# Kernel tuning notes

Hardware: AMD Instinct MI355X
Metric: run time of the kernel (lower is better)

Reference implementation:

```python
import jax, jax.numpy as jnp
import numpy as np

ALPHA = 0.5
E_MINUS_1 = float(np.e - 1.0)  # exp(1) - 1; exp(0) - 1 == 0

B = 4096
CLASSES = [128, 512, 2048, 8192]


def _ce(logits, labels):
    # mean cross-entropy: -mean(log_softmax(logits)[i, labels[i]])
    logp = jax.nn.log_softmax(logits, axis=-1)
    nll = -jnp.take_along_axis(logp, labels[:, None], axis=-1)[:, 0]
    return jnp.mean(nll)


def setup_inputs() -> dict:
    key = jax.random.key(0)
    ks = jax.random.split(key, 12)
    inp = {}
    for l, c in enumerate(CLASSES):
        inp[f"out{l}"] = jax.random.normal(ks[l], (B, c), dtype=jnp.float32)
    # targets[:, l] must be < CLASSES[l]; keep all < min(CLASSES) for simplicity
    inp["targets"] = jax.random.randint(ks[4], (B, 4), 0, 128).astype(jnp.int64)
    for l, c in enumerate(CLASSES):
        inp[f"pred{l}"] = jax.random.randint(ks[5 + l], (B,), 0, c).astype(jnp.int64)
    inp["valid01"] = jax.random.randint(ks[9], (128, 512), 0, 2).astype(bool)
    inp["valid12"] = jax.random.randint(ks[10], (512, 2048), 0, 2).astype(bool)
    inp["valid23"] = jax.random.randint(ks[11], (2048, 8192), 0, 2).astype(bool)
    return inp


def reference(out0, out1, out2, out3, targets, pred0, pred1, pred2, pred3,
              valid01, valid12, valid23):
    outputs = [out0, out1, out2, out3]
    preds = [pred0, pred1, pred2, pred3]
    valids = [valid01, valid12, valid23]

    total_ce = sum(_ce(outputs[l], targets[:, l]) for l in range(len(outputs)))

    # dependency loss: per sample, exp(D)-1 with D=0 if (prev_pred -> curr_pred)
    # is a valid parent-child pair, else D=1; averaged over batch, summed over levels
    total_dep = jnp.zeros((), dtype=out0.dtype)
    for l, V in enumerate(valids):
        ok = V[preds[l], preds[l + 1]]  # [B] bool gather (vectorized dict lookup)
        total_dep = total_dep + E_MINUS_1 * jnp.mean(1.0 - ok.astype(out0.dtype))

    total = ALPHA * total_ce + (1.0 - ALPHA) * total_dep
    return (total, total_ce, total_dep)
```

## Files before the change

### kernel.cpp

```cpp
#include <hip/hip_runtime.h>
#include <float.h>


#define NB 4096

static constexpr float LOG2E = 1.4426950408889634f;
static constexpr float LN2   = 0.6931471805599453f;
static constexpr float E_M1  = 1.7182818284590452f;

__device__ __forceinline__ float hw_exp2(float x) { return __builtin_amdgcn_exp2f(x); }
__device__ __forceinline__ float hw_log2(float x) { return __builtin_amdgcn_logf(x); }

__device__ __forceinline__ float wave_max(float v) {
    #pragma unroll
    for (int off = 32; off; off >>= 1) v = fmaxf(v, __shfl_xor(v, off));
    return v;
}
__device__ __forceinline__ float wave_sum(float v) {
    #pragma unroll
    for (int off = 32; off; off >>= 1) v += __shfl_xor(v, off);
    return v;
}
__device__ __forceinline__ float max4(float4 v) {
    return fmaxf(fmaxf(v.x, v.y), fmaxf(v.z, v.w));
}
__device__ __forceinline__ float sumexp4(float4 v, float M) {
    return hw_exp2((v.x - M) * LOG2E) + hw_exp2((v.y - M) * LOG2E)
         + hw_exp2((v.z - M) * LOG2E) + hw_exp2((v.w - M) * LOG2E);
}

__global__ __launch_bounds__(256) void ce_fused_kernel(
    const float* __restrict__ o0, const float* __restrict__ o1,
    const float* __restrict__ o2, const float* __restrict__ o3,
    const int* __restrict__ targets,
    const int* __restrict__ p0, const int* __restrict__ p1,
    const int* __restrict__ p2, const int* __restrict__ p3,
    const int* __restrict__ v01, const int* __restrict__ v12,
    const int* __restrict__ v23, float* __restrict__ ws8)
{
    const int row  = blockIdx.x;
    const int tid  = threadIdx.x;
    const int wv   = tid >> 6;
    const int lane = tid & 63;

    int ia = 0, ib = 0, ic = 0, id = 0;
    if (tid == 192) {
        ia = p0[row]; ib = p1[row]; ic = p2[row]; id = p3[row];
    }

    const float4* r3 = (const float4*)(o3 + (size_t)row * 8192);
    float4 v3[8];
    #pragma unroll
    for (int k = 0; k < 8; k++) v3[k] = r3[tid + (k << 8)];

    const float4* r0 = (const float4*)(o0 + (size_t)row * 128);
    const float4* r1 = (const float4*)(o1 + (size_t)row * 512);
    const float4* r2 = (const float4*)(o2 + (size_t)row * 2048);
    float4 vs[4];
    if (wv == 0) {
        if (lane < 32) vs[0] = r0[lane];
    } else if (wv == 1) {
        vs[0] = r1[lane];
        vs[1] = r1[lane + 64];
    } else {
        const int t2 = tid - 128;
        #pragma unroll
        for (int j = 0; j < 4; j++) vs[j] = r2[t2 + j * 128];
    }

    if (tid == 192) {
        const float ok0 = (v01[ia * 512  + ib] != 0) ? 1.f : 0.f;
        const float ok1 = (v12[ib * 2048 + ic] != 0) ? 1.f : 0.f;
        const float ok2 = (v23[ic * 8192 + id] != 0) ? 1.f : 0.f;
        ws8[row * 8 + 4] = ok0;
        ws8[row * 8 + 5] = ok1;
        ws8[row * 8 + 6] = ok2;
    }

    float xt_a = 0.0f, xt_b = 0.0f;
    if (tid == 0) {
        xt_a = o3[(size_t)row * 8192 + targets[row * 4 + 3]];
        xt_b = o0[(size_t)row * 128  + targets[row * 4 + 0]];
    } else if (tid == 64) {
        xt_a = o1[(size_t)row * 512  + targets[row * 4 + 1]];
    } else if (tid == 128) {
        xt_a = o2[(size_t)row * 2048 + targets[row * 4 + 2]];
    }

    __shared__ float lm3[4], lm2[2], ls3[4], ls2[2];

    float m3 = -FLT_MAX;
    #pragma unroll
    for (int k = 0; k < 8; k++) m3 = fmaxf(m3, max4(v3[k]));
    m3 = wave_max(m3);

    float msml = -FLT_MAX;
    if (wv == 0) {
        if (lane < 32) msml = max4(vs[0]);
    } else if (wv == 1) {
        msml = fmaxf(max4(vs[0]), max4(vs[1]));
    } else {
        #pragma unroll
        for (int j = 0; j < 4; j++) msml = fmaxf(msml, max4(vs[j]));
    }
    msml = wave_max(msml);

    if (lane == 0) {
        lm3[wv] = m3;
        if (wv >= 2) lm2[wv - 2] = msml;
    }
    __syncthreads();

    const float M3 = fmaxf(fmaxf(lm3[0], lm3[1]), fmaxf(lm3[2], lm3[3]));
    const float M2 = (wv >= 2) ? fmaxf(lm2[0], lm2[1]) : 0.0f;

    float s3 = 0.0f;
    #pragma unroll
    for (int k = 0; k < 8; k++) s3 += sumexp4(v3[k], M3);
    s3 = wave_sum(s3);

    float ssml = 0.0f;
    if (wv == 0) {
        if (lane < 32) ssml = sumexp4(vs[0], msml);
    } else if (wv == 1) {
        ssml = sumexp4(vs[0], msml) + sumexp4(vs[1], msml);
    } else {
        #pragma unroll
        for (int j = 0; j < 4; j++) ssml += sumexp4(vs[j], M2);
    }
    ssml = wave_sum(ssml);

    if (lane == 0) {
        ls3[wv] = s3;
        if (wv >= 2) ls2[wv - 2] = ssml;
    }
    __syncthreads();

    if (tid == 0) {
        const float S3 = ls3[0] + ls3[1] + ls3[2] + ls3[3];
        ws8[row * 8 + 3] = M3 + hw_log2(S3) * LN2 - xt_a;
        ws8[row * 8 + 0] = msml + hw_log2(ssml) * LN2 - xt_b;
    } else if (tid == 64) {
        ws8[row * 8 + 1] = msml + hw_log2(ssml) * LN2 - xt_a;
    } else if (tid == 128) {
        const float S2 = ls2[0] + ls2[1];
        ws8[row * 8 + 2] = M2 + hw_log2(S2) * LN2 - xt_a;
    }
}

__global__ __launch_bounds__(1024) void finalize_kernel(
    const float* __restrict__ ws8, float* __restrict__ out)
{
    const int tid = threadIdx.x;
    const float4* w4 = (const float4*)ws8;

    float c0 = 0.f, c1 = 0.f, c2 = 0.f, c3 = 0.f;
    float ok0 = 0.f, ok1 = 0.f, ok2 = 0.f;
    #pragma unroll
    for (int j = 0; j < 4; j++) {
        const int row = tid + j * 1024;
        float4 a = w4[row * 2];
        float4 b = w4[row * 2 + 1];
        c0 += a.x; c1 += a.y; c2 += a.z; c3 += a.w;
        ok0 += b.x; ok1 += b.y; ok2 += b.z;
    }

    float vals[7] = {c0, c1, c2, c3, ok0, ok1, ok2};
    #pragma unroll
    for (int q = 0; q < 7; q++) {
        #pragma unroll
        for (int off = 32; off; off >>= 1) vals[q] += __shfl_xor(vals[q], off);
    }
    __shared__ float lds[16][7];
    if ((tid & 63) == 0) {
        #pragma unroll
        for (int q = 0; q < 7; q++) lds[tid >> 6][q] = vals[q];
    }
    __syncthreads();

    if (tid == 0) {
        float res[7];
        #pragma unroll
        for (int q = 0; q < 7; q++) {
            float t = 0.f;
            for (int w = 0; w < 16; w++) t += lds[w][q];
            res[q] = t;
        }
        const float inv_b = 1.0f / (float)NB;
        const float total_ce = (res[0] + res[1] + res[2] + res[3]) * inv_b;
        float total_dep = 0.f;
        #pragma unroll
        for (int q = 4; q < 7; q++)
            total_dep += E_M1 * (((float)NB - res[q]) * inv_b);
        out[0] = 0.5f * total_ce + 0.5f * total_dep;
        out[1] = total_ce;
        out[2] = total_dep;
    }
}

extern "C" void kernel_launch(void* const* d_in, const int* in_sizes, int n_in,
                              void* d_out, int out_size, void* d_ws, size_t ws_size,
                              hipStream_t stream)
{
    const float* o0 = (const float*)d_in[0];
    const float* o1 = (const float*)d_in[1];
    const float* o2 = (const float*)d_in[2];
    const float* o3 = (const float*)d_in[3];
    const int* targets = (const int*)d_in[4];
    const int* p0 = (const int*)d_in[5];
    const int* p1 = (const int*)d_in[6];
    const int* p2 = (const int*)d_in[7];
    const int* p3 = (const int*)d_in[8];
    const int* v01 = (const int*)d_in[9];
    const int* v12 = (const int*)d_in[10];
    const int* v23 = (const int*)d_in[11];

    float* ws8 = (float*)d_ws;
    float* out = (float*)d_out;

    ce_fused_kernel<<<NB, 256, 0, stream>>>(o0, o1, o2, o3, targets,
                                            p0, p1, p2, p3, v01, v12, v23, ws8);
    finalize_kernel<<<1, 1024, 0, stream>>>(ws8, out);
}
```

Baseline: 269.5 us.

## Use online softmax with single barrier and staged row loads

Replaces the two-pass max-then-sum softmax reduction with an online (running max, rescaled sum) formulation combined across lanes, waves and the block. This removes one block barrier and halves the per-thread register buffer for the largest row by loading its second half after processing the first. It adds extra exp evaluations for rescaling and in the shuffle reductions, and the second-half loads may expose more memory latency.

```diff
diff --git a/kernel.cpp b/kernel.cpp
--- a/kernel.cpp
+++ b/kernel.cpp
@@ -11,22 +11,27 @@
 __device__ __forceinline__ float hw_exp2(float x) { return __builtin_amdgcn_exp2f(x); }
 __device__ __forceinline__ float hw_log2(float x) { return __builtin_amdgcn_logf(x); }
 
-__device__ __forceinline__ float wave_max(float v) {
-    #pragma unroll
-    for (int off = 32; off; off >>= 1) v = fmaxf(v, __shfl_xor(v, off));
-    return v;
-}
-__device__ __forceinline__ float wave_sum(float v) {
-    #pragma unroll
-    for (int off = 32; off; off >>= 1) v += __shfl_xor(v, off);
-    return v;
-}
 __device__ __forceinline__ float max4(float4 v) {
     return fmaxf(fmaxf(v.x, v.y), fmaxf(v.z, v.w));
 }
 __device__ __forceinline__ float sumexp4(float4 v, float M) {
     return hw_exp2((v.x - M) * LOG2E) + hw_exp2((v.y - M) * LOG2E)
          + hw_exp2((v.z - M) * LOG2E) + hw_exp2((v.w - M) * LOG2E);
+}
+__device__ __forceinline__ void online4(float4 v, float& m, float& s) {
+    float mn = fmaxf(m, max4(v));
+    s = s * hw_exp2((m - mn) * LOG2E) + sumexp4(v, mn);
+    m = mn;
+}
+__device__ __forceinline__ void combine_ms(float& m, float& s, float m2, float s2) {
+    float mn = fmaxf(m, m2);
+    s = s * hw_exp2((m - mn) * LOG2E) + s2 * hw_exp2((m2 - mn) * LOG2E);
+    m = mn;
+}
+__device__ __forceinline__ void wave_reduce_ms(float& m, float& s) {
+    #pragma unroll
+    for (int off = 32; off; off >>= 1)
+        combine_ms(m, s, __shfl_xor(m, off), __shfl_xor(s, off));
 }
 
 __global__ __launch_bounds__(256) void ce_fused_kernel(
@@ -49,32 +54,32 @@
     }
 
     const float4* r3 = (const float4*)(o3 + (size_t)row * 8192);
-    float4 v3[8];
-    #pragma unroll
-    for (int k = 0; k < 8; k++) v3[k] = r3[tid + (k << 8)];
+    float4 b0 = r3[tid];
+    float4 b1 = r3[tid + 256];
+    float4 b2 = r3[tid + 512];
+    float4 b3 = r3[tid + 768];
 
     const float4* r0 = (const float4*)(o0 + (size_t)row * 128);
     const float4* r1 = (const float4*)(o1 + (size_t)row * 512);
     const float4* r2 = (const float4*)(o2 + (size_t)row * 2048);
-    float4 vs[4];
+    float4 u0, u1, u2, u3;
     if (wv == 0) {
-        if (lane < 32) vs[0] = r0[lane];
+        if (lane < 32) u0 = r0[lane];
     } else if (wv == 1) {
-        vs[0] = r1[lane];
-        vs[1] = r1[lane + 64];
+        u0 = r1[lane];
+        u1 = r1[lane + 64];
     } else {
         const int t2 = tid - 128;
-        #pragma unroll
-        for (int j = 0; j < 4; j++) vs[j] = r2[t2 + j * 128];
+        u0 = r2[t2];
+        u1 = r2[t2 + 128];
+        u2 = r2[t2 + 256];
+        u3 = r2[t2 + 384];
     }
 
     if (tid == 192) {
-        const float ok0 = (v01[ia * 512  + ib] != 0) ? 1.f : 0.f;
-        const float ok1 = (v12[ib * 2048 + ic] != 0) ? 1.f : 0.f;
-        const float ok2 = (v23[ic * 8192 + id] != 0) ? 1.f : 0.f;
-        ws8[row * 8 + 4] = ok0;
-        ws8[row * 8 + 5] = ok1;
-        ws8[row * 8 + 6] = ok2;
+        ws8[row * 8 + 4] = (v01[ia * 512  + ib] != 0) ? 1.f : 0.f;
+        ws8[row * 8 + 5] = (v12[ib * 2048 + ic] != 0) ? 1.f : 0.f;
+        ws8[row * 8 + 6] = (v23[ic * 8192 + id] != 0) ? 1.f : 0.f;
     }
 
     float xt_a = 0.0f, xt_b = 0.0f;
@@ -87,64 +92,55 @@
         xt_a = o2[(size_t)row * 2048 + targets[row * 4 + 2]];
     }
 
-    __shared__ float lm3[4], lm2[2], ls3[4], ls2[2];
-
-    float m3 = -FLT_MAX;
-    #pragma unroll
-    for (int k = 0; k < 8; k++) m3 = fmaxf(m3, max4(v3[k]));
-    m3 = wave_max(m3);
-
-    float msml = -FLT_MAX;
+    float m0 = -FLT_MAX, m1 = -FLT_MAX, m2 = -FLT_MAX, m3 = -FLT_MAX;
+    float s0 = 0.f, s1 = 0.f, s2 = 0.f, s3 = 0.f;
+    online4(b0, m0, s0);  b0 = r3[tid + 1024];
+    online4(b1, m1, s1);  b1 = r3[tid + 1280];
+    online4(b2, m2, s2);  b2 = r3[tid + 1536];
+    online4(b3, m3, s3);  b3 = r3[tid + 1792];
+    online4(b0, m0, s0);
+    online4(b1, m1, s1);
+    online4(b2, m2, s2);
+    online4(b3, m3, s3);
+    combine_ms(m0, s0, m1, s1);
+    combine_ms(m2, s2, m3, s3);
+    combine_ms(m0, s0, m2, s2);
+    wave_reduce_ms(m0, s0);
+
+    float ms = -FLT_MAX, ss = 0.f;
     if (wv == 0) {
-        if (lane < 32) msml = max4(vs[0]);
+        if (lane < 32) online4(u0, ms, ss);
     } else if (wv == 1) {
-        msml = fmaxf(max4(vs[0]), max4(vs[1]));
+        online4(u0, ms, ss);
+        online4(u1, ms, ss);
     } else {
-        #pragma unroll
-        for (int j = 0; j < 4; j++) msml = fmaxf(msml, max4(vs[j]));
-    }
-    msml = wave_max(msml);
-
+        online4(u0, ms, ss);
+        online4(u1, ms, ss);
+        online4(u2, ms, ss);
+        online4(u3, ms, ss);
+    }
+    wave_reduce_ms(ms, ss);
+
+    __shared__ float lm3[4], ls3[4], lmS[2], lsS[2];
     if (lane == 0) {
-        lm3[wv] = m3;
-        if (wv >= 2) lm2[wv - 2] = msml;
+        lm3[wv] = m0; ls3[wv] = s0;
+        if (wv >= 2) { lmS[wv - 2] = ms; lsS[wv - 2] = ss; }
     }
     __syncthreads();
 
-    const float M3 = fmaxf(fmaxf(lm3[0], lm3[1]), fmaxf(lm3[2], lm3[3]));
-    const float M2 = (wv >= 2) ? fmaxf(lm2[0], lm2[1]) : 0.0f;
-
-    float s3 = 0.0f;
-    #pragma unroll
-    for (int k = 0; k < 8; k++) s3 += sumexp4(v3[k], M3);
-    s3 = wave_sum(s3);
-
-    float ssml = 0.0f;
-    if (wv == 0) {
-        if (lane < 32) ssml = sumexp4(vs[0], msml);
-    } else if (wv == 1) {
-        ssml = sumexp4(vs[0], msml) + sumexp4(vs[1], msml);
-    } else {
-        #pragma unroll
-        for (int j = 0; j < 4; j++) ssml += sumexp4(vs[j], M2);
-    }
-    ssml = wave_sum(ssml);
-
-    if (lane == 0) {
-        ls3[wv] = s3;
-        if (wv >= 2) ls2[wv - 2] = ssml;
-    }
-    __syncthreads();
-
     if (tid == 0) {
-        const float S3 = ls3[0] + ls3[1] + ls3[2] + ls3[3];
-        ws8[row * 8 + 3] = M3 + hw_log2(S3) * LN2 - xt_a;
-        ws8[row * 8 + 0] = msml + hw_log2(ssml) * LN2 - xt_b;
+        float M = lm3[0], S = ls3[0];
+        combine_ms(M, S, lm3[1], ls3[1]);
+        combine_ms(M, S, lm3[2], ls3[2]);
+        combine_ms(M, S, lm3[3], ls3[3]);
+        ws8[row * 8 + 3] = M + hw_log2(S) * LN2 - xt_a;
+        ws8[row * 8 + 0] = ms + hw_log2(ss) * LN2 - xt_b;
     } else if (tid == 64) {
-        ws8[row * 8 + 1] = msml + hw_log2(ssml) * LN2 - xt_a;
+        ws8[row * 8 + 1] = ms + hw_log2(ss) * LN2 - xt_a;
     } else if (tid == 128) {
-        const float S2 = ls2[0] + ls2[1];
-        ws8[row * 8 + 2] = M2 + hw_log2(S2) * LN2 - xt_a;
+        float M = lmS[0], S = lsS[0];
+        combine_ms(M, S, lmS[1], lsS[1]);
+        ws8[row * 8 + 2] = M + hw_log2(S) * LN2 - xt_a;
     }
 }
 
```

Result: no change. 273.8 us (+1.6%).

## Split per-row CE work into independent waves with online softmax for large rows

Applied to the files above, without the earlier changes.

The kernel no longer uses one 256-thread block per row. Each wave now handles one task: an 8192-wide row, a 2048-wide row, or the small 512 and 128 rows plus the dependency lookups. The 8192-wide rows use a single-pass online max/sum-exp with 8 independent accumulators and register double-buffered loads. This removes block-level __syncthreads and LDS reductions and aims for better load balance. In exchange, each wave streams 32 KB serially and does extra exp work for the online rescaling.

```diff
diff --git a/kernel.cpp b/kernel.cpp
--- a/kernel.cpp
+++ b/kernel.cpp
@@ -11,16 +11,6 @@
 __device__ __forceinline__ float hw_exp2(float x) { return __builtin_amdgcn_exp2f(x); }
 __device__ __forceinline__ float hw_log2(float x) { return __builtin_amdgcn_logf(x); }
 
-__device__ __forceinline__ float wave_max(float v) {
-    #pragma unroll
-    for (int off = 32; off; off >>= 1) v = fmaxf(v, __shfl_xor(v, off));
-    return v;
-}
-__device__ __forceinline__ float wave_sum(float v) {
-    #pragma unroll
-    for (int off = 32; off; off >>= 1) v += __shfl_xor(v, off);
-    return v;
-}
 __device__ __forceinline__ float max4(float4 v) {
     return fmaxf(fmaxf(v.x, v.y), fmaxf(v.z, v.w));
 }
@@ -28,8 +18,28 @@
     return hw_exp2((v.x - M) * LOG2E) + hw_exp2((v.y - M) * LOG2E)
          + hw_exp2((v.z - M) * LOG2E) + hw_exp2((v.w - M) * LOG2E);
 }
-
-__global__ __launch_bounds__(256) void ce_fused_kernel(
+__device__ __forceinline__ void online4(float4 v, float& m, float& s) {
+    float mn = fmaxf(m, max4(v));
+    s = s * hw_exp2((m - mn) * LOG2E) + sumexp4(v, mn);
+    m = mn;
+}
+__device__ __forceinline__ void combine_ms(float& m, float& s, float m2, float s2) {
+    float mn = fmaxf(m, m2);
+    s = s * hw_exp2((m - mn) * LOG2E) + s2 * hw_exp2((m2 - mn) * LOG2E);
+    m = mn;
+}
+__device__ __forceinline__ float wave_max(float v) {
+    #pragma unroll
+    for (int off = 32; off; off >>= 1) v = fmaxf(v, __shfl_xor(v, off));
+    return v;
+}
+__device__ __forceinline__ float wave_sum(float v) {
+    #pragma unroll
+    for (int off = 32; off; off >>= 1) v += __shfl_xor(v, off);
+    return v;
+}
+
+__global__ __launch_bounds__(256) void ce_wave_kernel(
     const float* __restrict__ o0, const float* __restrict__ o1,
     const float* __restrict__ o2, const float* __restrict__ o3,
     const int* __restrict__ targets,
@@ -38,113 +48,120 @@
     const int* __restrict__ v01, const int* __restrict__ v12,
     const int* __restrict__ v23, float* __restrict__ ws8)
 {
-    const int row  = blockIdx.x;
-    const int tid  = threadIdx.x;
-    const int wv   = tid >> 6;
-    const int lane = tid & 63;
-
-    int ia = 0, ib = 0, ic = 0, id = 0;
-    if (tid == 192) {
-        ia = p0[row]; ib = p1[row]; ic = p2[row]; id = p3[row];
-    }
-
-    const float4* r3 = (const float4*)(o3 + (size_t)row * 8192);
-    float4 v3[8];
-    #pragma unroll
-    for (int k = 0; k < 8; k++) v3[k] = r3[tid + (k << 8)];
-
-    const float4* r0 = (const float4*)(o0 + (size_t)row * 128);
-    const float4* r1 = (const float4*)(o1 + (size_t)row * 512);
-    const float4* r2 = (const float4*)(o2 + (size_t)row * 2048);
-    float4 vs[4];
-    if (wv == 0) {
-        if (lane < 32) vs[0] = r0[lane];
-    } else if (wv == 1) {
-        vs[0] = r1[lane];
-        vs[1] = r1[lane + 64];
+    const int gw   = (blockIdx.x << 2) | (threadIdx.x >> 6);
+    const int lane = threadIdx.x & 63;
+
+    if (gw < 4096) {
+        const int row = gw;
+        const float4* r3 = (const float4*)(o3 + (size_t)row * 8192);
+
+        int tgt = 0;
+        if (lane == 0) tgt = targets[row * 4 + 3];
+
+        float4 buf[8];
+        #pragma unroll
+        for (int j = 0; j < 8; j++) buf[j] = r3[lane + (j << 6)];
+
+        float xt = 0.0f;
+        if (lane == 0) xt = o3[(size_t)row * 8192 + tgt];
+
+        float m[8], s[8];
+        #pragma unroll
+        for (int j = 0; j < 8; j++) { m[j] = -FLT_MAX; s[j] = 0.0f; }
+
+        #pragma unroll
+        for (int r = 0; r < 3; r++) {
+            #pragma unroll
+            for (int j = 0; j < 8; j++) {
+                float4 v = buf[j];
+                buf[j] = r3[lane + (((r + 1) << 3 | j) << 6)];
+                online4(v, m[j], s[j]);
+            }
+        }
+        #pragma unroll
+        for (int j = 0; j < 8; j++) online4(buf[j], m[j], s[j]);
+
+        combine_ms(m[0], s[0], m[1], s[1]);
+        combine_ms(m[2], s[2], m[3], s[3]);
+        combine_ms(m[4], s[4], m[5], s[5]);
+        combine_ms(m[6], s[6], m[7], s[7]);
+        combine_ms(m[0], s[0], m[2], s[2]);
+        combine_ms(m[4], s[4], m[6], s[6]);
+        combine_ms(m[0], s[0], m[4], s[4]);
+        float M = m[0], S = s[0];
+        #pragma unroll
+        for (int off = 32; off; off >>= 1)
+            combine_ms(M, S, __shfl_xor(M, off), __shfl_xor(S, off));
+
+        if (lane == 0) ws8[row * 8 + 3] = M + hw_log2(S) * LN2 - xt;
+
+    } else if (gw < 8192) {
+        const int row = gw - 4096;
+        const float4* r2 = (const float4*)(o2 + (size_t)row * 2048);
+
+        int tgt = 0;
+        if (lane == 0) tgt = targets[row * 4 + 2];
+
+        float4 buf[8];
+        #pragma unroll
+        for (int j = 0; j < 8; j++) buf[j] = r2[lane + (j << 6)];
+
+        float xt = 0.0f;
+        if (lane == 0) xt = o2[(size_t)row * 2048 + tgt];
+
+        float pm = -FLT_MAX;
+        #pragma unroll
+        for (int j = 0; j < 8; j++) pm = fmaxf(pm, max4(buf[j]));
+        const float M = wave_max(pm);
+
+        float ps = 0.0f;
+        #pragma unroll
+        for (int j = 0; j < 8; j++) ps += sumexp4(buf[j], M);
+        const float S = wave_sum(ps);
+
+        if (lane == 0) ws8[row * 8 + 2] = M + hw_log2(S) * LN2 - xt;
+
     } else {
-        const int t2 = tid - 128;
-        #pragma unroll
-        for (int j = 0; j < 4; j++) vs[j] = r2[t2 + j * 128];
-    }
-
-    if (tid == 192) {
-        const float ok0 = (v01[ia * 512  + ib] != 0) ? 1.f : 0.f;
-        const float ok1 = (v12[ib * 2048 + ic] != 0) ? 1.f : 0.f;
-        const float ok2 = (v23[ic * 8192 + id] != 0) ? 1.f : 0.f;
-        ws8[row * 8 + 4] = ok0;
-        ws8[row * 8 + 5] = ok1;
-        ws8[row * 8 + 6] = ok2;
-    }
-
-    float xt_a = 0.0f, xt_b = 0.0f;
-    if (tid == 0) {
-        xt_a = o3[(size_t)row * 8192 + targets[row * 4 + 3]];
-        xt_b = o0[(size_t)row * 128  + targets[row * 4 + 0]];
-    } else if (tid == 64) {
-        xt_a = o1[(size_t)row * 512  + targets[row * 4 + 1]];
-    } else if (tid == 128) {
-        xt_a = o2[(size_t)row * 2048 + targets[row * 4 + 2]];
-    }
-
-    __shared__ float lm3[4], lm2[2], ls3[4], ls2[2];
-
-    float m3 = -FLT_MAX;
-    #pragma unroll
-    for (int k = 0; k < 8; k++) m3 = fmaxf(m3, max4(v3[k]));
-    m3 = wave_max(m3);
-
-    float msml = -FLT_MAX;
-    if (wv == 0) {
-        if (lane < 32) msml = max4(vs[0]);
-    } else if (wv == 1) {
-        msml = fmaxf(max4(vs[0]), max4(vs[1]));
-    } else {
-        #pragma unroll
-        for (int j = 0; j < 4; j++) msml = fmaxf(msml, max4(vs[j]));
-    }
-    msml = wave_max(msml);
-
-    if (lane == 0) {
-        lm3[wv] = m3;
-        if (wv >= 2) lm2[wv - 2] = msml;
-    }
-    __syncthreads();
-
-    const float M3 = fmaxf(fmaxf(lm3[0], lm3[1]), fmaxf(lm3[2], lm3[3]));
-    const float M2 = (wv >= 2) ? fmaxf(lm2[0], lm2[1]) : 0.0f;
-
-    float s3 = 0.0f;
-    #pragma unroll
-    for (int k = 0; k < 8; k++) s3 += sumexp4(v3[k], M3);
-    s3 = wave_sum(s3);
-
-    float ssml = 0.0f;
-    if (wv == 0) {
-        if (lane < 32) ssml = sumexp4(vs[0], msml);
-    } else if (wv == 1) {
-        ssml = sumexp4(vs[0], msml) + sumexp4(vs[1], msml);
-    } else {
-        #pragma unroll
-        for (int j = 0; j < 4; j++) ssml += sumexp4(vs[j], M2);
-    }
-    ssml = wave_sum(ssml);
-
-    if (lane == 0) {
-        ls3[wv] = s3;
-        if (wv >= 2) ls2[wv - 2] = ssml;
-    }
-    __syncthreads();
-
-    if (tid == 0) {
-        const float S3 = ls3[0] + ls3[1] + ls3[2] + ls3[3];
-        ws8[row * 8 + 3] = M3 + hw_log2(S3) * LN2 - xt_a;
-        ws8[row * 8 + 0] = msml + hw_log2(ssml) * LN2 - xt_b;
-    } else if (tid == 64) {
-        ws8[row * 8 + 1] = msml + hw_log2(ssml) * LN2 - xt_a;
-    } else if (tid == 128) {
-        const float S2 = ls2[0] + ls2[1];
-        ws8[row * 8 + 2] = M2 + hw_log2(S2) * LN2 - xt_a;
+        const int row = gw - 8192;
+
+        int ia = 0, ib = 0, ic = 0, id = 0;
+        int t1 = 0, t0 = 0;
+        if (lane == 0) {
+            ia = p0[row]; ib = p1[row]; ic = p2[row]; id = p3[row];
+            t1 = targets[row * 4 + 1];
+            t0 = targets[row * 4 + 0];
+        }
+
+        const float4* r1 = (const float4*)(o1 + (size_t)row * 512);
+        const float4* r0 = (const float4*)(o0 + (size_t)row * 128);
+        float4 u0 = r1[lane];
+        float4 u1 = r1[lane + 64];
+        float4 w0;
+        if (lane < 32) w0 = r0[lane];
+
+        float xt1 = 0.0f, xt0 = 0.0f;
+        if (lane == 0) {
+            xt1 = o1[(size_t)row * 512 + t1];
+            xt0 = o0[(size_t)row * 128 + t0];
+            ws8[row * 8 + 4] = (v01[ia * 512  + ib] != 0) ? 1.f : 0.f;
+            ws8[row * 8 + 5] = (v12[ib * 2048 + ic] != 0) ? 1.f : 0.f;
+            ws8[row * 8 + 6] = (v23[ic * 8192 + id] != 0) ? 1.f : 0.f;
+        }
+
+        float pm1 = fmaxf(max4(u0), max4(u1));
+        const float M1 = wave_max(pm1);
+        float ps1 = sumexp4(u0, M1) + sumexp4(u1, M1);
+        const float S1 = wave_sum(ps1);
+
+        float pm0 = (lane < 32) ? max4(w0) : -FLT_MAX;
+        const float M0 = wave_max(pm0);
+        float ps0 = (lane < 32) ? sumexp4(w0, M0) : 0.0f;
+        const float S0 = wave_sum(ps0);
+
+        if (lane == 0) {
+            ws8[row * 8 + 1] = M1 + hw_log2(S1) * LN2 - xt1;
+            ws8[row * 8 + 0] = M0 + hw_log2(S0) * LN2 - xt0;
+        }
     }
 }
 
@@ -218,7 +235,7 @@
     float* ws8 = (float*)d_ws;
     float* out = (float*)d_out;
 
-    ce_fused_kernel<<<NB, 256, 0, stream>>>(o0, o1, o2, o3, targets,
-                                            p0, p1, p2, p3, v01, v12, v23, ws8);
+    ce_wave_kernel<<<3072, 256, 0, stream>>>(o0, o1, o2, o3, targets,
+                                             p0, p1, p2, p3, v01, v12, v23, ws8);
     finalize_kernel<<<1, 1024, 0, stream>>>(ws8, out);
 }
```

New measurement: 268.6 us (median of 2 runs). Within noise of the previous version (-0.3%).
